# Kernel tuning notes

Hardware: AMD Instinct MI355X
Metric: run time of the kernel (lower is better)

## Reference

```python
import jax, jax.numpy as jnp
import numpy as np

N_ADAPTERS = 16
RANK = 16
ALPHA = 16.0
SCALING = ALPHA / RANK
B, S, IN, OUT = 32, 512, 1024, 4096


def setup_inputs() -> dict:
    key = jax.random.key(0)
    k1, k2, k3, k4, k5, k6 = jax.random.split(key, 6)
    hidden_states = jax.random.normal(k1, (B, S, IN), dtype=jnp.float32)
    adapter_ids = jax.random.randint(k2, (B,), 0, N_ADAPTERS, dtype=jnp.int64)
    W = jax.random.normal(k3, (IN, OUT), dtype=jnp.float32) * 0.02
    b = jax.random.normal(k4, (OUT,), dtype=jnp.float32) * 0.02
    lora_a = jax.random.normal(k5, (N_ADAPTERS, IN, RANK), dtype=jnp.float32) * (1.0 / np.sqrt(IN))
    lora_b = jax.random.normal(k6, (N_ADAPTERS, RANK, OUT), dtype=jnp.float32) * 0.02
    return {"hidden_states": hidden_states, "adapter_ids": adapter_ids,
            "W": W, "b": b, "lora_a": lora_a, "lora_b": lora_b}


def reference(hidden_states, adapter_ids, W, b, lora_a, lora_b):
    # Base Conv1D (GPT-2 style): x @ W + b  -> [B, S, OUT]
    base_output = jnp.einsum('bsi,io->bso', hidden_states, W) + b
    # Per-sample adapter gather (replaces the unique-id loop + boolean masks):
    a_sel = lora_a[adapter_ids]          # [B, IN, R]
    b_sel = lora_b[adapter_ids]          # [B, R, OUT]
    low_rank = jnp.einsum('bsi,bir->bsr', hidden_states, a_sel)   # [B, S, R]
    delta = jnp.einsum('bsr,bro->bso', low_rank, b_sel) * SCALING # [B, S, OUT]
    return base_output + delta
```

## Files before the change

### kernel.cpp

```cpp
#include <hip/hip_runtime.h>

#define M_TOT 16384
#define N_TOT 4096
#define K_TOT 1024
#define R_LORA 16
#define N_ADAPT 16

#define BM 128
#define BN 128
#define BK 64

typedef __attribute__((ext_vector_type(8))) short bf16x8_t;
typedef __attribute__((ext_vector_type(4))) float f32x4_t;

__device__ __forceinline__ unsigned short f2bf(float f) {
  unsigned u = __builtin_bit_cast(unsigned, f);
  u += 0x7FFFu + ((u >> 16) & 1u);
  return (unsigned short)(u >> 16);
}

__device__ __forceinline__ void gload_lds16(const void* g, void* l) {
  __builtin_amdgcn_global_load_lds(
      (const __attribute__((address_space(1))) unsigned int*)g,
      (__attribute__((address_space(3))) unsigned int*)l, 16, 0, 0);
}

__global__ __launch_bounds__(256) void conv_x_kernel(const float* __restrict__ x,
                                                     unsigned short* __restrict__ xB) {
  size_t i = (size_t)blockIdx.x * 256 + threadIdx.x;
  const size_t stride = (size_t)gridDim.x * 256;
  const size_t n4 = (size_t)M_TOT * K_TOT / 4;
  for (; i < n4; i += stride) {
    float4 v = ((const float4*)x)[i];
    ushort4 h;
    h.x = f2bf(v.x); h.y = f2bf(v.y); h.z = f2bf(v.z); h.w = f2bf(v.w);
    ((ushort4*)xB)[i] = h;
  }
}

__global__ __launch_bounds__(256) void conv_w_kernel(const float* __restrict__ W,
                                                     unsigned short* __restrict__ WtB) {
  __shared__ float lds[64][65];
  const int k0 = blockIdx.x * 64;
  const int n0 = blockIdx.y * 64;
  const int t = threadIdx.x;
  const int rr = t >> 4;
  const int cc = (t & 15) * 4;
#pragma unroll
  for (int i = 0; i < 4; ++i) {
    int row = i * 16 + rr;
    float4 v = *(const float4*)(W + (size_t)(k0 + row) * N_TOT + n0 + cc);
    lds[row][cc + 0] = v.x; lds[row][cc + 1] = v.y;
    lds[row][cc + 2] = v.z; lds[row][cc + 3] = v.w;
  }
  __syncthreads();
#pragma unroll
  for (int i = 0; i < 4; ++i) {
    int nrow = i * 16 + rr;
    ushort4 h;
    h.x = f2bf(lds[cc + 0][nrow]); h.y = f2bf(lds[cc + 1][nrow]);
    h.z = f2bf(lds[cc + 2][nrow]); h.w = f2bf(lds[cc + 3][nrow]);
    *(ushort4*)(WtB + (size_t)(n0 + nrow) * K_TOT + k0 + cc) = h;
  }
}

__global__ __launch_bounds__(256) void prep_small_kernel(const float* __restrict__ lora_a,
                                                         const float* __restrict__ lora_b,
                                                         unsigned short* __restrict__ AtB,
                                                         unsigned short* __restrict__ lbT) {
  const int bid = blockIdx.x;
  const int t = threadIdx.x;
  if (bid < 64) {
    int idx = bid * 256 + t;
    int aid = idx >> 10;
    int k = idx & 1023;
    const float* src = lora_a + (size_t)idx * 16;
#pragma unroll
    for (int q = 0; q < 4; ++q) {
      float4 v = ((const float4*)src)[q];
#pragma unroll
      for (int j = 0; j < 4; ++j) {
        int r = q * 4 + j;
        float val = (j == 0) ? v.x : (j == 1) ? v.y : (j == 2) ? v.z : v.w;
        AtB[(((size_t)aid * 16 + r) << 10) + k] = f2bf(val);
      }
    }
  } else {
    int idx = (bid - 64) * 256 + t;
    int aid = idx >> 12;
    int n = idx & 4095;
    unsigned short o[16];
#pragma unroll
    for (int r = 0; r < 16; ++r)
      o[r] = f2bf(lora_b[((size_t)aid * 16 + r) * N_TOT + n] * 1.0f );
    ushort4* dst = (ushort4*)(lbT + ((size_t)aid * N_TOT + n) * 16);
#pragma unroll
    for (int q = 0; q < 4; ++q) {
      ushort4 h; h.x = o[q*4+0]; h.y = o[q*4+1]; h.z = o[q*4+2]; h.w = o[q*4+3];
      dst[q] = h;
    }
  }
}

__global__ __launch_bounds__(256) void lowrank_kernel(const unsigned short* __restrict__ xB,
                                                      const unsigned short* __restrict__ AtB,
                                                      const int* __restrict__ aids,
                                                      unsigned short* __restrict__ lrB) {
  __shared__ char As[BM * BK * 2];
  const int blk = blockIdx.x;
  const int t = threadIdx.x;
  const int lane = t & 63;
  const int w = t >> 6;
  const int fr = lane & 15, fq = lane >> 4;
  const int aid = aids[blk >> 2];

  const unsigned short* aSrc[4];
  char* aDst[4];
#pragma unroll
  for (int r = 0; r < 4; ++r) {
    int off = (r * 256 + t) * 16;
    int row = off >> 7, cb = off & 127;
    int sb = cb ^ ((row & 7) << 4);
    aSrc[r] = xB + (size_t)(blk * BM + row) * K_TOT + (sb >> 1);
    aDst[r] = As + off;
  }
  const unsigned short* bBase = AtB + ((size_t)aid * 16 + fr) * K_TOT + fq * 8;

  f32x4_t acc[2];
  acc[0] = (f32x4_t){0.f, 0.f, 0.f, 0.f};
  acc[1] = (f32x4_t){0.f, 0.f, 0.f, 0.f};

  for (int kt = 0; kt < K_TOT / BK; ++kt) {
#pragma unroll
    for (int r = 0; r < 4; ++r) gload_lds16(aSrc[r] + kt * BK, aDst[r]);
    __syncthreads();
#pragma unroll
    for (int ks = 0; ks < 2; ++ks) {
      bf16x8_t bfr = *(const bf16x8_t*)(bBase + kt * BK + ks * 32);
#pragma unroll
      for (int m = 0; m < 2; ++m) {
        int row = w * 32 + m * 16 + fr;
        int cb = ks * 64 + fq * 16;
        bf16x8_t af = *(const bf16x8_t*)(As + row * 128 + (cb ^ ((row & 7) << 4)));
        acc[m] = __builtin_amdgcn_mfma_f32_16x16x32_bf16(af, bfr, acc[m], 0, 0, 0);
      }
    }
    __syncthreads();
  }
#pragma unroll
  for (int m = 0; m < 2; ++m) {
    int gm0 = blk * BM + w * 32 + m * 16 + fq * 4;
#pragma unroll
    for (int q = 0; q < 4; ++q)
      lrB[(size_t)(gm0 + q) * R_LORA + fr] = f2bf(acc[m][q]);
  }
}

__global__ __launch_bounds__(256) void gemm_kernel(const unsigned short* __restrict__ xB,
                                                   const unsigned short* __restrict__ WtB,
                                                   const unsigned short* __restrict__ lrB,
                                                   const unsigned short* __restrict__ lbT,
                                                   const float* __restrict__ bias,
                                                   const int* __restrict__ aids,
                                                   float* __restrict__ out) {
  __shared__ char smem[2 * BM * BK * 2];
  char* As = smem;
  char* Bs = smem + BM * BK * 2;

  const int orig = blockIdx.x;
  const int wg = (orig & 7) * (4096 / 8) + (orig >> 3);
  const int tn = wg & 31;
  const int tm = wg >> 5;

  const int t = threadIdx.x;
  const int lane = t & 63;
  const int w = t >> 6;
  const int wr = w >> 1, wc = w & 1;
  const int fr = lane & 15, fq = lane >> 4;

  const unsigned short* aSrc[4];
  const unsigned short* bSrc[4];
  char* aDst[4];
  char* bDst[4];
#pragma unroll
  for (int r = 0; r < 4; ++r) {
    int off = (r * 256 + t) * 16;
    int row = off >> 7, cb = off & 127;
    int sb = cb ^ ((row & 7) << 4);
    aSrc[r] = xB + (size_t)(tm * BM + row) * K_TOT + (sb >> 1);
    bSrc[r] = WtB + (size_t)(tn * BN + row) * K_TOT + (sb >> 1);
    aDst[r] = As + off;
    bDst[r] = Bs + off;
  }

  f32x4_t acc[4][4];
#pragma unroll
  for (int m = 0; m < 4; ++m)
#pragma unroll
    for (int n = 0; n < 4; ++n) acc[m][n] = (f32x4_t){0.f, 0.f, 0.f, 0.f};

  for (int kt = 0; kt < K_TOT / BK; ++kt) {
#pragma unroll
    for (int r = 0; r < 4; ++r) gload_lds16(aSrc[r] + kt * BK, aDst[r]);
#pragma unroll
    for (int r = 0; r < 4; ++r) gload_lds16(bSrc[r] + kt * BK, bDst[r]);
    __syncthreads();
#pragma unroll
    for (int ks = 0; ks < 2; ++ks) {
      bf16x8_t af[4], bf[4];
#pragma unroll
      for (int m = 0; m < 4; ++m) {
        int row = wr * 64 + m * 16 + fr;
        int cb = ks * 64 + fq * 16;
        af[m] = *(const bf16x8_t*)(As + row * 128 + (cb ^ ((row & 7) << 4)));
      }
#pragma unroll
      for (int n = 0; n < 4; ++n) {
        int row = wc * 64 + n * 16 + fr;
        int cb = ks * 64 + fq * 16;
        bf[n] = *(const bf16x8_t*)(Bs + row * 128 + (cb ^ ((row & 7) << 4)));
      }
#pragma unroll
      for (int m = 0; m < 4; ++m)
#pragma unroll
        for (int n = 0; n < 4; ++n)
          acc[m][n] = __builtin_amdgcn_mfma_f32_16x16x32_bf16(af[m], bf[n], acc[m][n], 0, 0, 0);
    }
    __syncthreads();
  }

  const int aid = aids[tm >> 2];
  bf16x8_t z8 = {0, 0, 0, 0, 0, 0, 0, 0};
  bf16x8_t lrf[4], lbf[4];
#pragma unroll
  for (int m = 0; m < 4; ++m) { lrf[m] = z8; lbf[m] = z8; }
  if (fq < 2) {
#pragma unroll
    for (int m = 0; m < 4; ++m)
      lrf[m] = *(const bf16x8_t*)(lrB + (size_t)(tm * BM + wr * 64 + m * 16 + fr) * R_LORA + fq * 8);
#pragma unroll
    for (int n = 0; n < 4; ++n)
      lbf[n] = *(const bf16x8_t*)(lbT + ((size_t)aid * N_TOT + tn * BN + wc * 64 + n * 16 + fr) * R_LORA + fq * 8);
  }
#pragma unroll
  for (int m = 0; m < 4; ++m)
#pragma unroll
    for (int n = 0; n < 4; ++n)
      acc[m][n] = __builtin_amdgcn_mfma_f32_16x16x32_bf16(lrf[m], lbf[n], acc[m][n], 0, 0, 0);

#pragma unroll
  for (int n = 0; n < 4; ++n) {
    int gn = tn * BN + wc * 64 + n * 16 + fr;
    float bv = bias[gn];
#pragma unroll
    for (int m = 0; m < 4; ++m) {
      int gm0 = tm * BM + wr * 64 + m * 16 + fq * 4;
      float* op = out + (size_t)gm0 * N_TOT + gn;
#pragma unroll
      for (int q = 0; q < 4; ++q) op[(size_t)q * N_TOT] = acc[m][n][q] + bv;
    }
  }
}

extern "C" void kernel_launch(void* const* d_in, const int* in_sizes, int n_in,
                              void* d_out, int out_size, void* d_ws, size_t ws_size,
                              hipStream_t stream) {
  const float* x      = (const float*)d_in[0];
  const int*   aids   = (const int*)d_in[1];
  const float* W      = (const float*)d_in[2];
  const float* bias   = (const float*)d_in[3];
  const float* lora_a = (const float*)d_in[4];
  const float* lora_b = (const float*)d_in[5];
  float* out = (float*)d_out;

  char* ws = (char*)d_ws;
  unsigned short* xB  = (unsigned short*)(ws);
  unsigned short* WtB = (unsigned short*)(ws + (size_t)32 * 1024 * 1024);
  unsigned short* lrB = (unsigned short*)(ws + (size_t)40 * 1024 * 1024);
  unsigned short* AtB = (unsigned short*)(ws + (size_t)40 * 1024 * 1024 + 512 * 1024);
  unsigned short* lbT = (unsigned short*)(ws + (size_t)41 * 1024 * 1024);

  conv_x_kernel<<<2048, 256, 0, stream>>>(x, xB);
  conv_w_kernel<<<dim3(16, 64), 256, 0, stream>>>(W, WtB);
  prep_small_kernel<<<320, 256, 0, stream>>>(lora_a, lora_b, AtB, lbT);
  lowrank_kernel<<<128, 256, 0, stream>>>(xB, AtB, aids, lrB);
  gemm_kernel<<<4096, 256, 0, stream>>>(xB, WtB, lrB, lbT, bias, aids, out);
}
```

Baseline: 247.4 us.

## Use 256x256 double-buffered 8-wave GEMM and merge prep kernels

The main GEMM moves from 128x128 tiles with 4 waves to 256x256 tiles with 8 waves. It uses a 128KB double-buffered LDS pipeline that prefetches the next K tile while the MFMAs run, adds raised wave priority around the MFMA blocks, and staggers the A and B loads across four sub-phases. This is meant to raise data reuse per tile and hide global-to-LDS latency. The three conversion kernels are also fused into a single prep launch to cut launch overhead. The risks are lower occupancy (one block per CU), fragile hand-written waitcnt and barrier sequencing, and a grid of 1024 blocks that may balance poorly across CUs.

```diff
diff --git a/kernel.cpp b/kernel.cpp
--- a/kernel.cpp
+++ b/kernel.cpp
@@ -4,11 +4,11 @@
 #define N_TOT 4096
 #define K_TOT 1024
 #define R_LORA 16
-#define N_ADAPT 16
-
-#define BM 128
-#define BN 128
+
+#define BM 256
+#define BN 256
 #define BK 64
+#define NT (K_TOT / BK)
 
 typedef __attribute__((ext_vector_type(8))) short bf16x8_t;
 typedef __attribute__((ext_vector_type(4))) float f32x4_t;
@@ -25,79 +25,80 @@
       (__attribute__((address_space(3))) unsigned int*)l, 16, 0, 0);
 }
 
-__global__ __launch_bounds__(256) void conv_x_kernel(const float* __restrict__ x,
-                                                     unsigned short* __restrict__ xB) {
-  size_t i = (size_t)blockIdx.x * 256 + threadIdx.x;
-  const size_t stride = (size_t)gridDim.x * 256;
-  const size_t n4 = (size_t)M_TOT * K_TOT / 4;
-  for (; i < n4; i += stride) {
-    float4 v = ((const float4*)x)[i];
-    ushort4 h;
-    h.x = f2bf(v.x); h.y = f2bf(v.y); h.z = f2bf(v.z); h.w = f2bf(v.w);
-    ((ushort4*)xB)[i] = h;
-  }
-}
-
-__global__ __launch_bounds__(256) void conv_w_kernel(const float* __restrict__ W,
-                                                     unsigned short* __restrict__ WtB) {
+__global__ __launch_bounds__(256) void prep_kernel(const float* __restrict__ x,
+                                                   const float* __restrict__ W,
+                                                   const float* __restrict__ lora_a,
+                                                   const float* __restrict__ lora_b,
+                                                   unsigned short* __restrict__ xB,
+                                                   unsigned short* __restrict__ WtB,
+                                                   unsigned short* __restrict__ AtB,
+                                                   unsigned short* __restrict__ lbT) {
   __shared__ float lds[64][65];
-  const int k0 = blockIdx.x * 64;
-  const int n0 = blockIdx.y * 64;
-  const int t = threadIdx.x;
-  const int rr = t >> 4;
-  const int cc = (t & 15) * 4;
-#pragma unroll
-  for (int i = 0; i < 4; ++i) {
-    int row = i * 16 + rr;
-    float4 v = *(const float4*)(W + (size_t)(k0 + row) * N_TOT + n0 + cc);
-    lds[row][cc + 0] = v.x; lds[row][cc + 1] = v.y;
-    lds[row][cc + 2] = v.z; lds[row][cc + 3] = v.w;
-  }
-  __syncthreads();
-#pragma unroll
-  for (int i = 0; i < 4; ++i) {
-    int nrow = i * 16 + rr;
-    ushort4 h;
-    h.x = f2bf(lds[cc + 0][nrow]); h.y = f2bf(lds[cc + 1][nrow]);
-    h.z = f2bf(lds[cc + 2][nrow]); h.w = f2bf(lds[cc + 3][nrow]);
-    *(ushort4*)(WtB + (size_t)(n0 + nrow) * K_TOT + k0 + cc) = h;
-  }
-}
-
-__global__ __launch_bounds__(256) void prep_small_kernel(const float* __restrict__ lora_a,
-                                                         const float* __restrict__ lora_b,
-                                                         unsigned short* __restrict__ AtB,
-                                                         unsigned short* __restrict__ lbT) {
   const int bid = blockIdx.x;
   const int t = threadIdx.x;
-  if (bid < 64) {
-    int idx = bid * 256 + t;
-    int aid = idx >> 10;
-    int k = idx & 1023;
-    const float* src = lora_a + (size_t)idx * 16;
-#pragma unroll
-    for (int q = 0; q < 4; ++q) {
-      float4 v = ((const float4*)src)[q];
-#pragma unroll
-      for (int j = 0; j < 4; ++j) {
-        int r = q * 4 + j;
-        float val = (j == 0) ? v.x : (j == 1) ? v.y : (j == 2) ? v.z : v.w;
-        AtB[(((size_t)aid * 16 + r) << 10) + k] = f2bf(val);
+  if (bid < 1024) {
+    size_t i = (size_t)bid * 256 + t;
+    const size_t stride = (size_t)1024 * 256;
+    const size_t n4 = (size_t)M_TOT * K_TOT / 4;
+    for (; i < n4; i += stride) {
+      float4 v = ((const float4*)x)[i];
+      ushort4 h;
+      h.x = f2bf(v.x); h.y = f2bf(v.y); h.z = f2bf(v.z); h.w = f2bf(v.w);
+      ((ushort4*)xB)[i] = h;
+    }
+  } else if (bid < 2048) {
+    const int v = bid - 1024;
+    const int k0 = (v & 15) * 64;
+    const int n0 = (v >> 4) * 64;
+    const int rr = t >> 4;
+    const int cc = (t & 15) * 4;
+#pragma unroll
+    for (int i = 0; i < 4; ++i) {
+      int row = i * 16 + rr;
+      float4 w4 = *(const float4*)(W + (size_t)(k0 + row) * N_TOT + n0 + cc);
+      lds[row][cc + 0] = w4.x; lds[row][cc + 1] = w4.y;
+      lds[row][cc + 2] = w4.z; lds[row][cc + 3] = w4.w;
+    }
+    __syncthreads();
+#pragma unroll
+    for (int i = 0; i < 4; ++i) {
+      int nrow = i * 16 + rr;
+      ushort4 h;
+      h.x = f2bf(lds[cc + 0][nrow]); h.y = f2bf(lds[cc + 1][nrow]);
+      h.z = f2bf(lds[cc + 2][nrow]); h.w = f2bf(lds[cc + 3][nrow]);
+      *(ushort4*)(WtB + (size_t)(n0 + nrow) * K_TOT + k0 + cc) = h;
+    }
+  } else {
+    const int b2 = bid - 2048;
+    if (b2 < 64) {
+      int idx = b2 * 256 + t;
+      int aid = idx >> 10;
+      int k = idx & 1023;
+      const float* src = lora_a + (size_t)idx * 16;
+#pragma unroll
+      for (int q = 0; q < 4; ++q) {
+        float4 v4 = ((const float4*)src)[q];
+#pragma unroll
+        for (int j = 0; j < 4; ++j) {
+          int r = q * 4 + j;
+          float val = (j == 0) ? v4.x : (j == 1) ? v4.y : (j == 2) ? v4.z : v4.w;
+          AtB[(((size_t)aid * 16 + r) << 10) + k] = f2bf(val);
+        }
       }
-    }
-  } else {
-    int idx = (bid - 64) * 256 + t;
-    int aid = idx >> 12;
-    int n = idx & 4095;
-    unsigned short o[16];
-#pragma unroll
-    for (int r = 0; r < 16; ++r)
-      o[r] = f2bf(lora_b[((size_t)aid * 16 + r) * N_TOT + n] * 1.0f );
-    ushort4* dst = (ushort4*)(lbT + ((size_t)aid * N_TOT + n) * 16);
-#pragma unroll
-    for (int q = 0; q < 4; ++q) {
-      ushort4 h; h.x = o[q*4+0]; h.y = o[q*4+1]; h.z = o[q*4+2]; h.w = o[q*4+3];
-      dst[q] = h;
+    } else {
+      int idx = (b2 - 64) * 256 + t;
+      int aid = idx >> 12;
+      int n = idx & 4095;
+      unsigned short o[16];
+#pragma unroll
+      for (int r = 0; r < 16; ++r)
+        o[r] = f2bf(lora_b[((size_t)aid * 16 + r) * N_TOT + n]);
+      ushort4* dst = (ushort4*)(lbT + ((size_t)aid * N_TOT + n) * 16);
+#pragma unroll
+      for (int q = 0; q < 4; ++q) {
+        ushort4 h; h.x = o[q*4+0]; h.y = o[q*4+1]; h.z = o[q*4+2]; h.w = o[q*4+3];
+        dst[q] = h;
+      }
     }
   }
 }
@@ -106,7 +107,7 @@
                                                       const unsigned short* __restrict__ AtB,
                                                       const int* __restrict__ aids,
                                                       unsigned short* __restrict__ lrB) {
-  __shared__ char As[BM * BK * 2];
+  __shared__ char As[128 * 128];
   const int blk = blockIdx.x;
   const int t = threadIdx.x;
   const int lane = t & 63;
@@ -121,7 +122,7 @@
     int off = (r * 256 + t) * 16;
     int row = off >> 7, cb = off & 127;
     int sb = cb ^ ((row & 7) << 4);
-    aSrc[r] = xB + (size_t)(blk * BM + row) * K_TOT + (sb >> 1);
+    aSrc[r] = xB + (size_t)(blk * 128 + row) * K_TOT + (sb >> 1);
     aDst[r] = As + off;
   }
   const unsigned short* bBase = AtB + ((size_t)aid * 16 + fr) * K_TOT + fq * 8;
@@ -130,13 +131,13 @@
   acc[0] = (f32x4_t){0.f, 0.f, 0.f, 0.f};
   acc[1] = (f32x4_t){0.f, 0.f, 0.f, 0.f};
 
-  for (int kt = 0; kt < K_TOT / BK; ++kt) {
-#pragma unroll
-    for (int r = 0; r < 4; ++r) gload_lds16(aSrc[r] + kt * BK, aDst[r]);
+  for (int kt = 0; kt < K_TOT / 64; ++kt) {
+#pragma unroll
+    for (int r = 0; r < 4; ++r) gload_lds16(aSrc[r] + kt * 64, aDst[r]);
     __syncthreads();
 #pragma unroll
     for (int ks = 0; ks < 2; ++ks) {
-      bf16x8_t bfr = *(const bf16x8_t*)(bBase + kt * BK + ks * 32);
+      bf16x8_t bfr = *(const bf16x8_t*)(bBase + kt * 64 + ks * 32);
 #pragma unroll
       for (int m = 0; m < 2; ++m) {
         int row = w * 32 + m * 16 + fr;
@@ -149,112 +150,165 @@
   }
 #pragma unroll
   for (int m = 0; m < 2; ++m) {
-    int gm0 = blk * BM + w * 32 + m * 16 + fq * 4;
+    int gm0 = blk * 128 + w * 32 + m * 16 + fq * 4;
 #pragma unroll
     for (int q = 0; q < 4; ++q)
       lrB[(size_t)(gm0 + q) * R_LORA + fr] = f2bf(acc[m][q]);
   }
 }
 
-__global__ __launch_bounds__(256) void gemm_kernel(const unsigned short* __restrict__ xB,
-                                                   const unsigned short* __restrict__ WtB,
-                                                   const unsigned short* __restrict__ lrB,
-                                                   const unsigned short* __restrict__ lbT,
-                                                   const float* __restrict__ bias,
-                                                   const int* __restrict__ aids,
-                                                   float* __restrict__ out) {
-  __shared__ char smem[2 * BM * BK * 2];
-  char* As = smem;
-  char* Bs = smem + BM * BK * 2;
+#define BAR() __builtin_amdgcn_s_barrier()
+#define WAIT_LGKM0() asm volatile("s_waitcnt lgkmcnt(0)" ::: "memory")
+
+#define STAGE_HALF(gbase, koff, ldsbase)                                   \
+  do {                                                                     \
+    gload_lds16((const char*)(gbase) + (koff), (ldsbase) + t * 16);        \
+    gload_lds16((const char*)(gbase) + 64 * 2048 + (koff),                 \
+                (ldsbase) + 8192 + t * 16);                                \
+  } while (0)
+
+#define LDA(MH)                                                            \
+  do {                                                                     \
+    _Pragma("unroll") for (int m = 0; m < 4; ++m)                          \
+      _Pragma("unroll") for (int ks = 0; ks < 2; ++ks)                     \
+        aF[m][ks] = *(const bf16x8_t*)(bufA + (MH) * 8192 + m * 2048 +     \
+                                       (laneA ^ (ks << 6)));               \
+  } while (0)
+
+#define LDB(NH)                                                            \
+  do {                                                                     \
+    _Pragma("unroll") for (int n = 0; n < 2; ++n)                          \
+      _Pragma("unroll") for (int ks = 0; ks < 2; ++ks)                     \
+        bF[NH][n][ks] = *(const bf16x8_t*)(bufB + (NH) * 4096 + n * 2048 + \
+                                           (laneA ^ (ks << 6)));           \
+  } while (0)
+
+#define MM(MH, NH)                                                         \
+  do {                                                                     \
+    __builtin_amdgcn_s_setprio(1);                                         \
+    _Pragma("unroll") for (int ks = 0; ks < 2; ++ks)                       \
+      _Pragma("unroll") for (int m = 0; m < 4; ++m)                        \
+        _Pragma("unroll") for (int n = 0; n < 2; ++n)                      \
+          acc[(MH) * 4 + m][(NH) * 2 + n] =                                \
+              __builtin_amdgcn_mfma_f32_16x16x32_bf16(                     \
+                  aF[m][ks], bF[NH][n][ks],                                \
+                  acc[(MH) * 4 + m][(NH) * 2 + n], 0, 0, 0);               \
+    __builtin_amdgcn_s_setprio(0);                                         \
+  } while (0)
+
+__global__ __launch_bounds__(512, 1) void gemm_kernel(
+    const unsigned short* __restrict__ xB, const unsigned short* __restrict__ WtB,
+    const unsigned short* __restrict__ lrB, const unsigned short* __restrict__ lbT,
+    const float* __restrict__ bias, const int* __restrict__ aids,
+    float* __restrict__ out) {
+  __shared__ char smem[131072];
 
   const int orig = blockIdx.x;
-  const int wg = (orig & 7) * (4096 / 8) + (orig >> 3);
-  const int tn = wg & 31;
-  const int tm = wg >> 5;
+  const int wg = (orig & 7) * 128 + (orig >> 3);
+  const int tn = wg & 15;
+  const int tm = wg >> 4;
 
   const int t = threadIdx.x;
   const int lane = t & 63;
-  const int w = t >> 6;
-  const int wr = w >> 1, wc = w & 1;
+  const int wid = t >> 6;
+  const int wr = wid >> 2;
+  const int wc = wid & 3;
   const int fr = lane & 15, fq = lane >> 4;
 
-  const unsigned short* aSrc[4];
-  const unsigned short* bSrc[4];
-  char* aDst[4];
-  char* bDst[4];
-#pragma unroll
-  for (int r = 0; r < 4; ++r) {
-    int off = (r * 256 + t) * 16;
-    int row = off >> 7, cb = off & 127;
-    int sb = cb ^ ((row & 7) << 4);
-    aSrc[r] = xB + (size_t)(tm * BM + row) * K_TOT + (sb >> 1);
-    bSrc[r] = WtB + (size_t)(tn * BN + row) * K_TOT + (sb >> 1);
-    aDst[r] = As + off;
-    bDst[r] = Bs + off;
-  }
-
-  f32x4_t acc[4][4];
-#pragma unroll
-  for (int m = 0; m < 4; ++m)
+  const int laneA = fr * 128 + (((fq << 4) ^ ((fr & 7) << 4)));
+  const int waveAoff = wr * 16384;
+  const int waveBoff = 32768 + (wc >> 1) * 16384 + (wc & 1) * 8192;
+
+  const int srow = t >> 3;
+  const int sb = (((t & 7) ^ (srow & 7)) << 4);
+  const char* pAsrc0 = (const char*)xB + (size_t)(tm * 256 + srow) * 2048 + sb;
+  const char* pAsrc1 = pAsrc0 + (size_t)128 * 2048;
+  const char* pBsrc0 = (const char*)WtB + (size_t)(tn * 256 + srow) * 2048 + sb;
+  const char* pBsrc1 = pBsrc0 + (size_t)128 * 2048;
+
+  f32x4_t acc[8][4];
+#pragma unroll
+  for (int m = 0; m < 8; ++m)
 #pragma unroll
     for (int n = 0; n < 4; ++n) acc[m][n] = (f32x4_t){0.f, 0.f, 0.f, 0.f};
 
-  for (int kt = 0; kt < K_TOT / BK; ++kt) {
-#pragma unroll
-    for (int r = 0; r < 4; ++r) gload_lds16(aSrc[r] + kt * BK, aDst[r]);
-#pragma unroll
-    for (int r = 0; r < 4; ++r) gload_lds16(bSrc[r] + kt * BK, bDst[r]);
-    __syncthreads();
-#pragma unroll
-    for (int ks = 0; ks < 2; ++ks) {
-      bf16x8_t af[4], bf[4];
-#pragma unroll
-      for (int m = 0; m < 4; ++m) {
-        int row = wr * 64 + m * 16 + fr;
-        int cb = ks * 64 + fq * 16;
-        af[m] = *(const bf16x8_t*)(As + row * 128 + (cb ^ ((row & 7) << 4)));
-      }
-#pragma unroll
-      for (int n = 0; n < 4; ++n) {
-        int row = wc * 64 + n * 16 + fr;
-        int cb = ks * 64 + fq * 16;
-        bf[n] = *(const bf16x8_t*)(Bs + row * 128 + (cb ^ ((row & 7) << 4)));
-      }
-#pragma unroll
-      for (int m = 0; m < 4; ++m)
-#pragma unroll
-        for (int n = 0; n < 4; ++n)
-          acc[m][n] = __builtin_amdgcn_mfma_f32_16x16x32_bf16(af[m], bf[n], acc[m][n], 0, 0, 0);
-    }
-    __syncthreads();
-  }
-
-  const int aid = aids[tm >> 2];
-  bf16x8_t z8 = {0, 0, 0, 0, 0, 0, 0, 0};
-  bf16x8_t lrf[4], lbf[4];
-#pragma unroll
-  for (int m = 0; m < 4; ++m) { lrf[m] = z8; lbf[m] = z8; }
+  bf16x8_t aF[4][2];
+  bf16x8_t bF[2][2][2];
+
+  STAGE_HALF(pAsrc0, 0, smem + 0);
+  STAGE_HALF(pAsrc1, 0, smem + 16384);
+  STAGE_HALF(pBsrc0, 0, smem + 32768);
+  STAGE_HALF(pBsrc1, 0, smem + 49152);
+  STAGE_HALF(pBsrc0, 128, smem + 65536 + 32768);
+  STAGE_HALF(pBsrc1, 128, smem + 65536 + 49152);
+  asm volatile("s_waitcnt vmcnt(4)" ::: "memory");
+  BAR();
+
+#pragma unroll 1
+  for (int kt = 0; kt < NT; ++kt) {
+    char* base = smem + ((kt & 1) << 16);
+    char* nbase = smem + (((kt + 1) & 1) << 16);
+    char* bufA = base + waveAoff;
+    char* bufB = base + waveBoff;
+    const int kb1 = (kt + 1) * 128;
+    const int kb2 = (kt + 2) * 128;
+
+    LDA(0);
+    LDB(0);
+    if (kt + 1 < NT) STAGE_HALF(pAsrc0, kb1, nbase + 0);
+    asm volatile("s_waitcnt lgkmcnt(8)" ::: "memory");
+    BAR(); WAIT_LGKM0();
+    MM(0, 0);
+    BAR();
+
+    LDB(1);
+    if (kt + 1 < NT) STAGE_HALF(pAsrc1, kb1, nbase + 16384);
+    BAR(); WAIT_LGKM0();
+    MM(0, 1);
+    BAR();
+
+    LDA(1);
+    if (kt + 2 < NT) STAGE_HALF(pBsrc0, kb2, base + 32768);
+    BAR(); WAIT_LGKM0();
+    MM(1, 1);
+    BAR();
+
+    if (kt + 2 < NT) STAGE_HALF(pBsrc1, kb2, base + 49152);
+    BAR(); WAIT_LGKM0();
+    MM(1, 0);
+    if (kt < NT - 2) asm volatile("s_waitcnt vmcnt(4)" ::: "memory");
+    else             asm volatile("s_waitcnt vmcnt(0)" ::: "memory");
+    BAR();
+  }
+
+  const int aid = aids[tm >> 1];
+  bf16x8_t z8 = (bf16x8_t){0, 0, 0, 0, 0, 0, 0, 0};
+  bf16x8_t lrf[8], lbf[4];
+#pragma unroll
+  for (int m = 0; m < 8; ++m) lrf[m] = z8;
+#pragma unroll
+  for (int n = 0; n < 4; ++n) lbf[n] = z8;
   if (fq < 2) {
 #pragma unroll
-    for (int m = 0; m < 4; ++m)
-      lrf[m] = *(const bf16x8_t*)(lrB + (size_t)(tm * BM + wr * 64 + m * 16 + fr) * R_LORA + fq * 8);
+    for (int m = 0; m < 8; ++m)
+      lrf[m] = *(const bf16x8_t*)(lrB + (size_t)(tm * 256 + wr * 128 + m * 16 + fr) * R_LORA + fq * 8);
 #pragma unroll
     for (int n = 0; n < 4; ++n)
-      lbf[n] = *(const bf16x8_t*)(lbT + ((size_t)aid * N_TOT + tn * BN + wc * 64 + n * 16 + fr) * R_LORA + fq * 8);
-  }
-#pragma unroll
-  for (int m = 0; m < 4; ++m)
+      lbf[n] = *(const bf16x8_t*)(lbT + ((size_t)aid * N_TOT + tn * 256 + wc * 64 + n * 16 + fr) * R_LORA + fq * 8);
+  }
+#pragma unroll
+  for (int m = 0; m < 8; ++m)
 #pragma unroll
     for (int n = 0; n < 4; ++n)
       acc[m][n] = __builtin_amdgcn_mfma_f32_16x16x32_bf16(lrf[m], lbf[n], acc[m][n], 0, 0, 0);
 
 #pragma unroll
   for (int n = 0; n < 4; ++n) {
-    int gn = tn * BN + wc * 64 + n * 16 + fr;
+    int gn = tn * 256 + wc * 64 + n * 16 + fr;
     float bv = bias[gn];
 #pragma unroll
-    for (int m = 0; m < 4; ++m) {
-      int gm0 = tm * BM + wr * 64 + m * 16 + fq * 4;
+    for (int m = 0; m < 8; ++m) {
+      int gm0 = tm * 256 + wr * 128 + m * 16 + fq * 4;
       float* op = out + (size_t)gm0 * N_TOT + gn;
 #pragma unroll
       for (int q = 0; q < 4; ++q) op[(size_t)q * N_TOT] = acc[m][n][q] + bv;
@@ -280,9 +334,7 @@
   unsigned short* AtB = (unsigned short*)(ws + (size_t)40 * 1024 * 1024 + 512 * 1024);
   unsigned short* lbT = (unsigned short*)(ws + (size_t)41 * 1024 * 1024);
 
-  conv_x_kernel<<<2048, 256, 0, stream>>>(x, xB);
-  conv_w_kernel<<<dim3(16, 64), 256, 0, stream>>>(W, WtB);
-  prep_small_kernel<<<320, 256, 0, stream>>>(lora_a, lora_b, AtB, lbT);
+  prep_kernel<<<2368, 256, 0, stream>>>(x, W, lora_a, lora_b, xB, WtB, AtB, lbT);
   lowrank_kernel<<<128, 256, 0, stream>>>(xB, AtB, aids, lrB);
-  gemm_kernel<<<4096, 256, 0, stream>>>(xB, WtB, lrB, lbT, bias, aids, out);
-}
+  gemm_kernel<<<1024, 512, 0, stream>>>(xB, WtB, lrB, lbT, bias, aids, out);
+}
```

After: 213.3 us. 1.16x faster.
